# Optimization experiments

Hardware: AMD Instinct MI355X
Metric: run time of the kernel (lower is better)

The kernel has to match this reference:

```python
import jax, jax.numpy as jnp
import numpy as np
import math

NUM_HEADS = 8
DROPOUT_RATE = 0.1
D_IN = 32
D_PROJ = 32 * 16  # 512
B, SQ, SK = 8, 2048, 2048


def setup_inputs() -> dict:
    key = jax.random.key(0)
    ks = jax.random.split(key, 10)
    inv = 1.0 / math.sqrt(D_IN)
    return {
        "query": jax.random.normal(ks[0], (B, SQ, D_IN), dtype=jnp.float32),
        "key": jax.random.normal(ks[1], (B, SK, D_IN), dtype=jnp.float32),
        "value": jax.random.normal(ks[2], (B, SK, D_IN), dtype=jnp.float32),
        "mask": jax.random.randint(ks[3], (B, 1, 1, SK), 0, 2, dtype=jnp.int32),
        "Wq": jax.random.normal(ks[4], (D_PROJ, D_IN), dtype=jnp.float32) * inv,
        "bq": jax.random.normal(ks[5], (D_PROJ,), dtype=jnp.float32) * 0.02,
        "Wk": jax.random.normal(ks[6], (D_PROJ, D_IN), dtype=jnp.float32) * inv,
        "bk": jax.random.normal(ks[7], (D_PROJ,), dtype=jnp.float32) * 0.02,
        "Wv": jax.random.normal(ks[8], (D_PROJ, D_IN), dtype=jnp.float32) * inv,
        "bv": jax.random.normal(ks[9], (D_PROJ,), dtype=jnp.float32) * 0.02,
    }


def _split_heads(x):
    # [B, S, H*D] -> [B, H, S, D]
    b, s, _ = x.shape
    return x.reshape(b, s, NUM_HEADS, D_PROJ // NUM_HEADS).transpose(0, 2, 1, 3)


def reference(query, key, value, mask, Wq, bq, Wk, bk, Wv, bv):
    q = _split_heads(query @ Wq.T + bq)   # [B, H, Sq, D]
    k = _split_heads(key @ Wk.T + bk)     # [B, H, Sk, D]
    v = _split_heads(value @ Wv.T + bv)   # [B, H, Sk, D]

    head_dim = q.shape[-1]
    # mask only feeds this scalar; max(1-p, (1-p)/(Sm2*Sm3)) == 1-p for Sm2*Sm3 >= 1
    keep = 1.0 - DROPOUT_RATE
    scale_factor = jnp.maximum(jnp.float32(keep),
                               jnp.float32(keep / (mask.shape[2] * mask.shape[3])))

    scores = jnp.einsum("bhqd,bhkd->bhqk", q, k) * (scale_factor / math.sqrt(head_dim))
    probs = jax.nn.softmax(scores, axis=-1)
    # dropout treated as identity (eval mode) for a deterministic reference
    out = jnp.einsum("bhqk,bhkd->bhqd", probs, v)  # [B, H, Sq, D]
    b, h, sq, d = out.shape
    return out.transpose(0, 2, 1, 3).reshape(b, sq, h * d)
```

## Files before the change

### kernel.cpp

```cpp
#include <hip/hip_runtime.h>
#include <hip/hip_bf16.h>
#include <math.h>

#define B_   8
#define H_   8
#define S_   2048
#define D_   64
#define BH_  64
#define DPROJ_ 512

typedef __attribute__((ext_vector_type(8)))  _Float16 f16x8;
typedef __attribute__((ext_vector_type(4)))  float    f32x4;
typedef __attribute__((ext_vector_type(16))) float    f32x16;
typedef __attribute__((ext_vector_type(4)))  int      i32x4;

static __device__ __forceinline__ short f16bits(float f) {
    return __builtin_bit_cast(short, (_Float16)f);
}

static __device__ __forceinline__ f16x8 load8_f32_f16(const float* p) {
    const float4 a = ((const float4*)p)[0];
    const float4 b = ((const float4*)p)[1];
    f16x8 r;
    r[0] = (_Float16)a.x; r[1] = (_Float16)a.y; r[2] = (_Float16)a.z; r[3] = (_Float16)a.w;
    r[4] = (_Float16)b.x; r[5] = (_Float16)b.y; r[6] = (_Float16)b.z; r[7] = (_Float16)b.w;
    return r;
}

#if __has_builtin(__builtin_amdgcn_exp2f)
#define EXP2(x) __builtin_amdgcn_exp2f(x)
#else
#define EXP2(x) exp2f(x)
#endif

static __device__ __forceinline__ void pl32swap(unsigned int& a, unsigned int& b) {
#if __has_builtin(__builtin_amdgcn_permlane32_swap)
    auto r = __builtin_amdgcn_permlane32_swap((int)a, (int)b, false, false);
    a = (unsigned int)r[0];
    b = (unsigned int)r[1];
#else
    const bool lh0 = ((threadIdx.x & 63) < 32);
    unsigned int xa = (unsigned int)__shfl_xor((int)a, 32);
    unsigned int xb = (unsigned int)__shfl_xor((int)b, 32);
    unsigned int na = lh0 ? a : xb;
    unsigned int nb = lh0 ? xa : b;
    a = na; b = nb;
#endif
}

#define QKST 520

__global__ __launch_bounds__(256)
void proj_kernel(const float* __restrict__ query, const float* __restrict__ key,
                 const float* __restrict__ value,
                 const float* __restrict__ Wq, const float* __restrict__ bq,
                 const float* __restrict__ Wk, const float* __restrict__ bk,
                 const float* __restrict__ Wv, const float* __restrict__ bv,
                 short* __restrict__ qws, short* __restrict__ kws,
                 short* __restrict__ vws)
{
    __shared__ __align__(16) short shbuf[16384];

    const int tid  = threadIdx.x;
    const int wave = tid >> 6;
    const int lane = tid & 63;
    const int n    = lane & 15;
    const int quad = lane >> 4;
    const int kind = blockIdx.y;

    if (kind < 2) {
        short* tile = shbuf;
        const int r0   = blockIdx.x * 16;
        const int b    = r0 >> 11;
        const int s0   = r0 & 2047;
        const float QS = 0.16230319188537014f;

        const float* X    = kind ? key : query;
        const float* W    = kind ? Wk  : Wq;
        const float* bias = kind ? bk  : bq;
        short*       ows  = kind ? kws : qws;

        f16x8 af = load8_f32_f16(X + (r0 + n) * 32 + quad * 8);
        #pragma unroll
        for (int i = 0; i < 8; ++i) {
            const int c0 = wave * 128 + i * 16;
            f16x8 bfr = load8_f32_f16(W + (c0 + n) * 32 + quad * 8);
            f32x4 acc = {0.f, 0.f, 0.f, 0.f};
            acc = __builtin_amdgcn_mfma_f32_16x16x32_f16(af, bfr, acc, 0, 0, 0);
            const int c = c0 + n;
            const float bsf = bias[c];
            #pragma unroll
            for (int r = 0; r < 4; ++r) {
                float v = acc[r] + bsf;
                if (kind == 0) v *= QS;
                tile[(quad * 4 + r) * QKST + c] = f16bits(v);
            }
        }
        __syncthreads();

        #pragma unroll
        for (int k = 0; k < 4; ++k) {
            const int slot = k * 256 + tid;
            const int li   = slot & 7;
            const int chunk= slot >> 3;
            const int row  = chunk & 15;
            const int h    = chunk >> 4;
            uint4 vv = *(const uint4*)(tile + row * QKST + h * 64 + li * 8);
            *(uint4*)(ows + ((size_t)(b * 8 + h) * S_ + s0 + row) * 64 + li * 8) = vv;
        }
    } else {
        if (blockIdx.x >= 256) return;
        short* vtile = shbuf;
        const int r0   = blockIdx.x * 64;
        const int b    = r0 >> 11;
        const int s0   = r0 & 2047;
        const int sub  = wave >> 1;
        const int sh   = (wave & 1) * 16;

        #pragma unroll
        for (int half = 0; half < 2; ++half) {
            const int cbh = half * 256;
            f16x8 bfr = load8_f32_f16(value + (r0 + sub * 32 + sh + n) * 32 + quad * 8);
            #pragma unroll
            for (int i = 0; i < 16; ++i) {
                const int c0 = cbh + i * 16;
                f16x8 af = load8_f32_f16(Wv + (c0 + n) * 32 + quad * 8);
                f32x4 acc = {0.f, 0.f, 0.f, 0.f};
                acc = __builtin_amdgcn_mfma_f32_16x16x32_f16(af, bfr, acc, 0, 0, 0);
                #pragma unroll
                for (int r = 0; r < 4; ++r) {
                    const int dc = c0 + quad * 4 + r;
                    float v = acc[r] + bv[dc];
                    vtile[(sub * 256 + (dc - cbh)) * 32 + sh + n] = f16bits(v);
                }
            }
            __syncthreads();

            #pragma unroll
            for (int k = 0; k < 8; ++k) {
                const int slot = k * 256 + tid;
                const int li   = slot & 3;
                const int cl   = (slot >> 2) & 255;
                const int sb   = slot >> 10;
                const int c    = cbh + cl;
                const int bh   = b * 8 + (c >> 6);
                const int d    = c & 63;
                const int stile= (s0 >> 5) + sb;
                uint4 vv = *(const uint4*)(vtile + (sb * 256 + cl) * 32 + li * 8);
                *(uint4*)(vws + (((size_t)bh * (S_ / 32) + stile) * 64 + d) * 32 + li * 8) = vv;
            }
            if (half == 0) __syncthreads();
        }
    }
}

#define KST 72
#define VST 40
#define OTS 36

__global__ __launch_bounds__(256, 3)
void flash_kernel(const short* __restrict__ qws, const short* __restrict__ kws,
                  const short* __restrict__ vws, float* __restrict__ out)
{
    __shared__ __align__(16) short ldsk[2 * 32 * KST];
    __shared__ __align__(16) short ldsv[2 * 64 * VST];
    __shared__ __align__(16) float olds[4 * 32 * OTS];

    const int tid  = threadIdx.x;
    const int wave = tid >> 6;
    const int lane = tid & 63;
    const int m32  = lane & 31;
    const int lh   = lane >> 5;
    const int koff = lh * 8;
    const int bh   = blockIdx.x;
    const int q0   = blockIdx.y * 256 + wave * 64;

    const short* qbase = qws + (size_t)bh * S_ * D_;
    const short* kbase = kws + (size_t)bh * S_ * D_;
    const short* vbase = vws + (size_t)bh * (S_ / 32) * 2048;

    short* kdst0 = ldsk + (tid >> 3) * KST + (tid & 7) * 8;
    short* vdst0 = ldsv + (tid >> 2) * VST + (tid & 3) * 8;

    f16x8 qb[2][4];
    #pragma unroll
    for (int qg = 0; qg < 2; ++qg)
        #pragma unroll
        for (int h = 0; h < 4; ++h)
            qb[qg][h] = *(const f16x8*)(qbase + (q0 + qg * 32 + m32) * D_ + h * 16 + koff);

    f32x16 z16;
    #pragma unroll
    for (int r = 0; r < 16; ++r) z16[r] = 0.f;

    f32x16 o[2][2];
    float  pl[2] = {0.f, 0.f};
    #pragma unroll
    for (int qg = 0; qg < 2; ++qg)
        #pragma unroll
        for (int t = 0; t < 2; ++t)
            o[qg][t] = z16;

    {
        uint4 kr = *(const uint4*)(kbase + (size_t)tid * 8);
        uint4 vr = *(const uint4*)(vbase + (size_t)tid * 8);
        *(uint4*)kdst0 = kr;
        *(uint4*)vdst0 = vr;
    }
    __syncthreads();

    for (int it = 0; it < 64; ++it) {
        const int cur = it & 1, nx = cur ^ 1;

        uint4 kr, vr;
        if (it < 63) {
            kr = *(const uint4*)(kbase + (size_t)(it + 1) * 2048 + tid * 8);
            vr = *(const uint4*)(vbase + (size_t)(it + 1) * 2048 + tid * 8);
        }

        const short* kl = ldsk + cur * (32 * KST);
        const short* vl = ldsv + cur * (64 * VST);
        f16x8 kf[4], va[4];
        #pragma unroll
        for (int h = 0; h < 4; ++h)
            kf[h] = *(const f16x8*)(kl + m32 * KST + h * 16 + koff);
        #pragma unroll
        for (int t = 0; t < 2; ++t)
            #pragma unroll
            for (int kh = 0; kh < 2; ++kh)
                va[t * 2 + kh] = *(const f16x8*)(vl + (t * 32 + m32) * VST + kh * 16 + koff);

        #pragma unroll
        for (int qg = 0; qg < 2; ++qg) {
            f32x16 st = __builtin_amdgcn_mfma_f32_32x32x16_f16(kf[0], qb[qg][0], z16, 0, 0, 0);
            #pragma unroll
            for (int h = 1; h < 4; ++h)
                st = __builtin_amdgcn_mfma_f32_32x32x16_f16(kf[h], qb[qg][h], st, 0, 0, 0);

            float p[16];
            #pragma unroll
            for (int r = 0; r < 16; ++r) p[r] = EXP2(st[r]);
            float s01 = (p[0]+p[1]) + (p[2]+p[3]);
            float s23 = (p[4]+p[5]) + (p[6]+p[7]);
            float s45 = (p[8]+p[9]) + (p[10]+p[11]);
            float s67 = (p[12]+p[13]) + (p[14]+p[15]);
            pl[qg] += (s01 + s23) + (s45 + s67);

            unsigned int pk[8];
            #pragma unroll
            for (int i = 0; i < 8; ++i)
                pk[i] = __builtin_bit_cast(unsigned int,
                          __builtin_amdgcn_cvt_pkrtz(p[2 * i], p[2 * i + 1]));
            pl32swap(pk[0], pk[2]);
            pl32swap(pk[1], pk[3]);
            pl32swap(pk[4], pk[6]);
            pl32swap(pk[5], pk[7]);

            i32x4 bi0, bi1;
            bi0[0] = (int)pk[0]; bi0[1] = (int)pk[1];
            bi0[2] = (int)pk[2]; bi0[3] = (int)pk[3];
            bi1[0] = (int)pk[4]; bi1[1] = (int)pk[5];
            bi1[2] = (int)pk[6]; bi1[3] = (int)pk[7];
            f16x8 bf0 = __builtin_bit_cast(f16x8, bi0);
            f16x8 bf1 = __builtin_bit_cast(f16x8, bi1);

            #pragma unroll
            for (int t = 0; t < 2; ++t) {
                o[qg][t] = __builtin_amdgcn_mfma_f32_32x32x16_f16(va[t * 2 + 0], bf0, o[qg][t], 0, 0, 0);
                o[qg][t] = __builtin_amdgcn_mfma_f32_32x32x16_f16(va[t * 2 + 1], bf1, o[qg][t], 0, 0, 0);
            }
        }

        if (it < 63) {
            *(uint4*)(kdst0 + nx * (32 * KST)) = kr;
            *(uint4*)(vdst0 + nx * (64 * VST)) = vr;
        }
        __syncthreads();
    }

    const int b = bh >> 3, h = bh & 7;
    float* ow = olds + wave * (32 * OTS);
    #pragma unroll
    for (int qg = 0; qg < 2; ++qg) {
        float rs = pl[qg] + __shfl_xor(pl[qg], 32);
        float rl = 1.0f / rs;
        #pragma unroll
        for (int t = 0; t < 2; ++t) {
            const f32x16& ot = o[qg][t];
            #pragma unroll
            for (int g = 0; g < 4; ++g) {
                f32x4 w;
                w[0] = ot[g * 4 + 0] * rl;
                w[1] = ot[g * 4 + 1] * rl;
                w[2] = ot[g * 4 + 2] * rl;
                w[3] = ot[g * 4 + 3] * rl;
                *(f32x4*)(ow + m32 * OTS + 8 * g + 4 * lh) = w;
            }
            #pragma unroll
            for (int c = 0; c < 4; ++c) {
                const int row = (lane >> 3) + 8 * c;
                f32x4 v = *(const f32x4*)(ow + row * OTS + (lane & 7) * 4);
                const int sq = q0 + qg * 32 + row;
                *(f32x4*)(out + ((size_t)(b * S_ + sq)) * DPROJ_
                              + h * 64 + t * 32 + (lane & 7) * 4) = v;
            }
        }
    }
}

extern "C" void kernel_launch(void* const* d_in, const int* in_sizes, int n_in,
                              void* d_out, int out_size, void* d_ws, size_t ws_size,
                              hipStream_t stream)
{
    const float* query = (const float*)d_in[0];
    const float* key   = (const float*)d_in[1];
    const float* value = (const float*)d_in[2];
    const float* Wq = (const float*)d_in[4];
    const float* bq = (const float*)d_in[5];
    const float* Wk = (const float*)d_in[6];
    const float* bk = (const float*)d_in[7];
    const float* Wv = (const float*)d_in[8];
    const float* bv = (const float*)d_in[9];

    float* out = (float*)d_out;
    short* ws  = (short*)d_ws;
    const size_t TSZ = (size_t)BH_ * S_ * D_;
    short* qws = ws;
    short* kws = ws + TSZ;
    short* vws = ws + 2 * TSZ;

    proj_kernel<<<dim3((B_ * S_) / 16, 3), 256, 0, stream>>>(
        query, key, value, Wq, bq, Wk, bk, Wv, bv, qws, kws, vws);
    flash_kernel<<<dim3(BH_, S_ / 256), 256, 0, stream>>>(qws, kws, vws, out);
}
```

Measured before the change: 188.9 us.

## Triple-buffer K/V in LDS and register-prefetch next tile fragments

Turns the double-buffered K/V LDS pipeline into a three-stage ring. Global loads are issued two iterations ahead, and the next tile's K/V fragments are read from LDS into registers while the current tile's MFMAs run. The loop is unrolled by two so the register fragment sets can alternate. The aim is to hide global and LDS latency behind compute. In exchange it uses more LDS and registers, and launch bounds drop occupancy from 3 to 2 blocks per CU.

```diff
diff --git a/kernel.cpp b/kernel.cpp
--- a/kernel.cpp
+++ b/kernel.cpp
@@ -158,12 +158,97 @@
 #define VST 40
 #define OTS 36
 
-__global__ __launch_bounds__(256, 3)
+static __device__ __forceinline__ void flash_step(
+    int it,
+    const short* __restrict__ kbase, const short* __restrict__ vbase,
+    const short* ldsk, const short* ldsv,
+    short* kdst0, short* vdst0,
+    int m32, int koff, int tid,
+    int& rOff, int& wOff, int& fOff,
+    f16x8 (&kfc)[4], f16x8 (&vac)[4],
+    f16x8 (&kfn)[4], f16x8 (&van)[4],
+    const f16x8 (&qb)[2][4], const f32x16& z16,
+    f32x16 (&o)[2][2], float (&pl)[2])
+{
+    const bool doStage = (it < 62);
+    const bool doNext  = (it < 63);
+
+    uint4 kr, vr;
+    if (doStage) {
+        const size_t tb = (size_t)(it + 2) * 2048 + tid * 8;
+        kr = *(const uint4*)(kbase + tb);
+        vr = *(const uint4*)(vbase + tb);
+    }
+
+    if (doNext) {
+        const short* kl = ldsk + rOff * (32 * KST);
+        const short* vl = ldsv + rOff * (64 * VST);
+        #pragma unroll
+        for (int h = 0; h < 4; ++h)
+            kfn[h] = *(const f16x8*)(kl + m32 * KST + h * 16 + koff);
+        #pragma unroll
+        for (int t = 0; t < 2; ++t)
+            #pragma unroll
+            for (int kh = 0; kh < 2; ++kh)
+                van[t * 2 + kh] = *(const f16x8*)(vl + (t * 32 + m32) * VST + kh * 16 + koff);
+    }
+
+    #pragma unroll
+    for (int qg = 0; qg < 2; ++qg) {
+        f32x16 st = __builtin_amdgcn_mfma_f32_32x32x16_f16(kfc[0], qb[qg][0], z16, 0, 0, 0);
+        #pragma unroll
+        for (int h = 1; h < 4; ++h)
+            st = __builtin_amdgcn_mfma_f32_32x32x16_f16(kfc[h], qb[qg][h], st, 0, 0, 0);
+
+        float p[16];
+        #pragma unroll
+        for (int r = 0; r < 16; ++r) p[r] = EXP2(st[r]);
+        float s01 = (p[0]+p[1]) + (p[2]+p[3]);
+        float s23 = (p[4]+p[5]) + (p[6]+p[7]);
+        float s45 = (p[8]+p[9]) + (p[10]+p[11]);
+        float s67 = (p[12]+p[13]) + (p[14]+p[15]);
+        pl[qg] += (s01 + s23) + (s45 + s67);
+
+        unsigned int pk[8];
+        #pragma unroll
+        for (int i = 0; i < 8; ++i)
+            pk[i] = __builtin_bit_cast(unsigned int,
+                      __builtin_amdgcn_cvt_pkrtz(p[2 * i], p[2 * i + 1]));
+        pl32swap(pk[0], pk[2]);
+        pl32swap(pk[1], pk[3]);
+        pl32swap(pk[4], pk[6]);
+        pl32swap(pk[5], pk[7]);
+
+        i32x4 bi0, bi1;
+        bi0[0] = (int)pk[0]; bi0[1] = (int)pk[1];
+        bi0[2] = (int)pk[2]; bi0[3] = (int)pk[3];
+        bi1[0] = (int)pk[4]; bi1[1] = (int)pk[5];
+        bi1[2] = (int)pk[6]; bi1[3] = (int)pk[7];
+        f16x8 bf0 = __builtin_bit_cast(f16x8, bi0);
+        f16x8 bf1 = __builtin_bit_cast(f16x8, bi1);
+
+        #pragma unroll
+        for (int t = 0; t < 2; ++t) {
+            o[qg][t] = __builtin_amdgcn_mfma_f32_32x32x16_f16(vac[t * 2 + 0], bf0, o[qg][t], 0, 0, 0);
+            o[qg][t] = __builtin_amdgcn_mfma_f32_32x32x16_f16(vac[t * 2 + 1], bf1, o[qg][t], 0, 0, 0);
+        }
+    }
+
+    if (doStage) {
+        *(uint4*)(kdst0 + wOff * (32 * KST)) = kr;
+        *(uint4*)(vdst0 + wOff * (64 * VST)) = vr;
+    }
+    __syncthreads();
+
+    int t_ = fOff; fOff = rOff; rOff = wOff; wOff = t_;
+}
+
+__global__ __launch_bounds__(256, 2)
 void flash_kernel(const short* __restrict__ qws, const short* __restrict__ kws,
                   const short* __restrict__ vws, float* __restrict__ out)
 {
-    __shared__ __align__(16) short ldsk[2 * 32 * KST];
-    __shared__ __align__(16) short ldsv[2 * 64 * VST];
+    __shared__ __align__(16) short ldsk[3 * 32 * KST];
+    __shared__ __align__(16) short ldsv[3 * 64 * VST];
     __shared__ __align__(16) float olds[4 * 32 * OTS];
 
     const int tid  = threadIdx.x;
@@ -202,80 +287,36 @@
             o[qg][t] = z16;
 
     {
-        uint4 kr = *(const uint4*)(kbase + (size_t)tid * 8);
-        uint4 vr = *(const uint4*)(vbase + (size_t)tid * 8);
-        *(uint4*)kdst0 = kr;
-        *(uint4*)vdst0 = vr;
+        uint4 k0 = *(const uint4*)(kbase + (size_t)tid * 8);
+        uint4 v0 = *(const uint4*)(vbase + (size_t)tid * 8);
+        uint4 k1 = *(const uint4*)(kbase + (size_t)2048 + tid * 8);
+        uint4 v1 = *(const uint4*)(vbase + (size_t)2048 + tid * 8);
+        *(uint4*)kdst0 = k0;
+        *(uint4*)vdst0 = v0;
+        *(uint4*)(kdst0 + 32 * KST) = k1;
+        *(uint4*)(vdst0 + 64 * VST) = v1;
     }
     __syncthreads();
 
-    for (int it = 0; it < 64; ++it) {
-        const int cur = it & 1, nx = cur ^ 1;
-
-        uint4 kr, vr;
-        if (it < 63) {
-            kr = *(const uint4*)(kbase + (size_t)(it + 1) * 2048 + tid * 8);
-            vr = *(const uint4*)(vbase + (size_t)(it + 1) * 2048 + tid * 8);
-        }
-
-        const short* kl = ldsk + cur * (32 * KST);
-        const short* vl = ldsv + cur * (64 * VST);
-        f16x8 kf[4], va[4];
-        #pragma unroll
-        for (int h = 0; h < 4; ++h)
-            kf[h] = *(const f16x8*)(kl + m32 * KST + h * 16 + koff);
-        #pragma unroll
-        for (int t = 0; t < 2; ++t)
-            #pragma unroll
-            for (int kh = 0; kh < 2; ++kh)
-                va[t * 2 + kh] = *(const f16x8*)(vl + (t * 32 + m32) * VST + kh * 16 + koff);
-
-        #pragma unroll
-        for (int qg = 0; qg < 2; ++qg) {
-            f32x16 st = __builtin_amdgcn_mfma_f32_32x32x16_f16(kf[0], qb[qg][0], z16, 0, 0, 0);
-            #pragma unroll
-            for (int h = 1; h < 4; ++h)
-                st = __builtin_amdgcn_mfma_f32_32x32x16_f16(kf[h], qb[qg][h], st, 0, 0, 0);
-
-            float p[16];
-            #pragma unroll
-            for (int r = 0; r < 16; ++r) p[r] = EXP2(st[r]);
-            float s01 = (p[0]+p[1]) + (p[2]+p[3]);
-            float s23 = (p[4]+p[5]) + (p[6]+p[7]);
-            float s45 = (p[8]+p[9]) + (p[10]+p[11]);
-            float s67 = (p[12]+p[13]) + (p[14]+p[15]);
-            pl[qg] += (s01 + s23) + (s45 + s67);
-
-            unsigned int pk[8];
-            #pragma unroll
-            for (int i = 0; i < 8; ++i)
-                pk[i] = __builtin_bit_cast(unsigned int,
-                          __builtin_amdgcn_cvt_pkrtz(p[2 * i], p[2 * i + 1]));
-            pl32swap(pk[0], pk[2]);
-            pl32swap(pk[1], pk[3]);
-            pl32swap(pk[4], pk[6]);
-            pl32swap(pk[5], pk[7]);
-
-            i32x4 bi0, bi1;
-            bi0[0] = (int)pk[0]; bi0[1] = (int)pk[1];
-            bi0[2] = (int)pk[2]; bi0[3] = (int)pk[3];
-            bi1[0] = (int)pk[4]; bi1[1] = (int)pk[5];
-            bi1[2] = (int)pk[6]; bi1[3] = (int)pk[7];
-            f16x8 bf0 = __builtin_bit_cast(f16x8, bi0);
-            f16x8 bf1 = __builtin_bit_cast(f16x8, bi1);
-
-            #pragma unroll
-            for (int t = 0; t < 2; ++t) {
-                o[qg][t] = __builtin_amdgcn_mfma_f32_32x32x16_f16(va[t * 2 + 0], bf0, o[qg][t], 0, 0, 0);
-                o[qg][t] = __builtin_amdgcn_mfma_f32_32x32x16_f16(va[t * 2 + 1], bf1, o[qg][t], 0, 0, 0);
-            }
-        }
-
-        if (it < 63) {
-            *(uint4*)(kdst0 + nx * (32 * KST)) = kr;
-            *(uint4*)(vdst0 + nx * (64 * VST)) = vr;
-        }
-        __syncthreads();
+    f16x8 kfA[4], vaA[4], kfB[4], vaB[4];
+    #pragma unroll
+    for (int h = 0; h < 4; ++h)
+        kfA[h] = *(const f16x8*)(ldsk + m32 * KST + h * 16 + koff);
+    #pragma unroll
+    for (int t = 0; t < 2; ++t)
+        #pragma unroll
+        for (int kh = 0; kh < 2; ++kh)
+            vaA[t * 2 + kh] = *(const f16x8*)(ldsv + (t * 32 + m32) * VST + kh * 16 + koff);
+
+    int rOff = 1, wOff = 2, fOff = 0;
+
+    for (int it = 0; it < 64; it += 2) {
+        flash_step(it,     kbase, vbase, ldsk, ldsv, kdst0, vdst0,
+                   m32, koff, tid, rOff, wOff, fOff,
+                   kfA, vaA, kfB, vaB, qb, z16, o, pl);
+        flash_step(it + 1, kbase, vbase, ldsk, ldsv, kdst0, vdst0,
+                   m32, koff, tid, rOff, wOff, fOff,
+                   kfB, vaB, kfA, vaA, qb, z16, o, pl);
     }
 
     const int b = bh >> 3, h = bh & 7;
```

After: 185.0 us. -2.0%, faster.

## Pre-swizzle K/V into MFMA fragment order and load directly from global memory

Applied to the files above, without the earlier changes.

The projection kernel now writes K and V into a fragment-ordered layout so each lane can fetch its MFMA operands with contiguous 16-byte global loads. The flash kernel drops the LDS double buffer and its per-iteration __syncthreads, and instead register-double-buffers K/V fragments across two unrolled iterations. Launch bounds drop to 2 blocks per SM to leave room for the extra registers. Each wave now fetches K/V itself instead of sharing an LDS copy across the four waves, which raises L2 traffic and lowers occupancy.

```diff
diff --git a/kernel.cpp b/kernel.cpp
--- a/kernel.cpp
+++ b/kernel.cpp
@@ -104,9 +104,16 @@
             const int li   = slot & 7;
             const int chunk= slot >> 3;
             const int row  = chunk & 15;
-            const int h    = chunk >> 4;
-            uint4 vv = *(const uint4*)(tile + row * QKST + h * 64 + li * 8);
-            *(uint4*)(ows + ((size_t)(b * 8 + h) * S_ + s0 + row) * 64 + li * 8) = vv;
+            const int hd   = chunk >> 4;
+            uint4 vv = *(const uint4*)(tile + row * QKST + hd * 64 + li * 8);
+            const int bh = b * 8 + hd;
+            if (kind == 0) {
+                *(uint4*)(ows + ((size_t)bh * S_ + s0 + row) * 64 + li * 8) = vv;
+            } else {
+                const int s = s0 + row;
+                *(uint4*)(ows + (size_t)bh * (S_ * 64)
+                              + (size_t)(s >> 5) * 2048 + li * 256 + (s & 31) * 8) = vv;
+            }
         }
     } else {
         if (blockIdx.x >= 256) return;
@@ -147,23 +154,69 @@
                 const int d    = c & 63;
                 const int stile= (s0 >> 5) + sb;
                 uint4 vv = *(const uint4*)(vtile + (sb * 256 + cl) * 32 + li * 8);
-                *(uint4*)(vws + (((size_t)bh * (S_ / 32) + stile) * 64 + d) * 32 + li * 8) = vv;
+                *(uint4*)(vws + (size_t)bh * (S_ * 64)
+                              + (size_t)stile * 2048
+                              + ((d >> 5) * 4 + (li >> 1) * 2 + (li & 1)) * 256
+                              + (d & 31) * 8) = vv;
             }
             if (half == 0) __syncthreads();
         }
     }
 }
 
-#define KST 72
-#define VST 40
 #define OTS 36
 
-__global__ __launch_bounds__(256, 3)
+static __device__ __forceinline__ void flash_compute(
+    const f16x8 (&kf)[4], const f16x8 (&va)[4],
+    const f16x8 (&qb)[2][4], const f32x16& z16,
+    f32x16 (&o)[2][2], float (&pl)[2])
+{
+    #pragma unroll
+    for (int qg = 0; qg < 2; ++qg) {
+        f32x16 st = __builtin_amdgcn_mfma_f32_32x32x16_f16(kf[0], qb[qg][0], z16, 0, 0, 0);
+        #pragma unroll
+        for (int h = 1; h < 4; ++h)
+            st = __builtin_amdgcn_mfma_f32_32x32x16_f16(kf[h], qb[qg][h], st, 0, 0, 0);
+
+        float p[16];
+        #pragma unroll
+        for (int r = 0; r < 16; ++r) p[r] = EXP2(st[r]);
+        float s01 = (p[0]+p[1]) + (p[2]+p[3]);
+        float s23 = (p[4]+p[5]) + (p[6]+p[7]);
+        float s45 = (p[8]+p[9]) + (p[10]+p[11]);
+        float s67 = (p[12]+p[13]) + (p[14]+p[15]);
+        pl[qg] += (s01 + s23) + (s45 + s67);
+
+        unsigned int pk[8];
+        #pragma unroll
+        for (int i = 0; i < 8; ++i)
+            pk[i] = __builtin_bit_cast(unsigned int,
+                      __builtin_amdgcn_cvt_pkrtz(p[2 * i], p[2 * i + 1]));
+        pl32swap(pk[0], pk[2]);
+        pl32swap(pk[1], pk[3]);
+        pl32swap(pk[4], pk[6]);
+        pl32swap(pk[5], pk[7]);
+
+        i32x4 bi0, bi1;
+        bi0[0] = (int)pk[0]; bi0[1] = (int)pk[1];
+        bi0[2] = (int)pk[2]; bi0[3] = (int)pk[3];
+        bi1[0] = (int)pk[4]; bi1[1] = (int)pk[5];
+        bi1[2] = (int)pk[6]; bi1[3] = (int)pk[7];
+        f16x8 bf0 = __builtin_bit_cast(f16x8, bi0);
+        f16x8 bf1 = __builtin_bit_cast(f16x8, bi1);
+
+        #pragma unroll
+        for (int t = 0; t < 2; ++t) {
+            o[qg][t] = __builtin_amdgcn_mfma_f32_32x32x16_f16(va[t * 2 + 0], bf0, o[qg][t], 0, 0, 0);
+            o[qg][t] = __builtin_amdgcn_mfma_f32_32x32x16_f16(va[t * 2 + 1], bf1, o[qg][t], 0, 0, 0);
+        }
+    }
+}
+
+__global__ __launch_bounds__(256, 2)
 void flash_kernel(const short* __restrict__ qws, const short* __restrict__ kws,
                   const short* __restrict__ vws, float* __restrict__ out)
 {
-    __shared__ __align__(16) short ldsk[2 * 32 * KST];
-    __shared__ __align__(16) short ldsv[2 * 64 * VST];
     __shared__ __align__(16) float olds[4 * 32 * OTS];
 
     const int tid  = threadIdx.x;
@@ -176,11 +229,9 @@
     const int q0   = blockIdx.y * 256 + wave * 64;
 
     const short* qbase = qws + (size_t)bh * S_ * D_;
-    const short* kbase = kws + (size_t)bh * S_ * D_;
-    const short* vbase = vws + (size_t)bh * (S_ / 32) * 2048;
-
-    short* kdst0 = ldsk + (tid >> 3) * KST + (tid & 7) * 8;
-    short* vdst0 = ldsv + (tid >> 2) * VST + (tid & 3) * 8;
+    const short* kfb   = kws + (size_t)bh * (S_ * 64);
+    const short* vfb   = vws + (size_t)bh * (S_ * 64);
+    const int loff = lh * 256 + m32 * 8;
 
     f16x8 qb[2][4];
     #pragma unroll
@@ -201,82 +252,30 @@
         for (int t = 0; t < 2; ++t)
             o[qg][t] = z16;
 
-    {
-        uint4 kr = *(const uint4*)(kbase + (size_t)tid * 8);
-        uint4 vr = *(const uint4*)(vbase + (size_t)tid * 8);
-        *(uint4*)kdst0 = kr;
-        *(uint4*)vdst0 = vr;
+    #define LOADFRAGS(T, kf, va) do {                                        \
+        const short* kp_ = kfb + (size_t)(T) * 2048 + loff;                  \
+        const short* vp_ = vfb + (size_t)(T) * 2048 + loff;                  \
+        kf[0] = *(const f16x8*)(kp_);                                        \
+        kf[1] = *(const f16x8*)(kp_ + 512);                                  \
+        kf[2] = *(const f16x8*)(kp_ + 1024);                                 \
+        kf[3] = *(const f16x8*)(kp_ + 1536);                                 \
+        va[0] = *(const f16x8*)(vp_);                                        \
+        va[1] = *(const f16x8*)(vp_ + 512);                                  \
+        va[2] = *(const f16x8*)(vp_ + 1024);                                 \
+        va[3] = *(const f16x8*)(vp_ + 1536);                                 \
+    } while (0)
+
+    f16x8 kfA[4], vaA[4], kfB[4], vaB[4];
+    LOADFRAGS(0, kfA, vaA);
+
+    for (int it = 0; it < 64; it += 2) {
+        LOADFRAGS(it + 1, kfB, vaB);
+        flash_compute(kfA, vaA, qb, z16, o, pl);
+        if (it + 2 < 64)
+            LOADFRAGS(it + 2, kfA, vaA);
+        flash_compute(kfB, vaB, qb, z16, o, pl);
     }
-    __syncthreads();
-
-    for (int it = 0; it < 64; ++it) {
-        const int cur = it & 1, nx = cur ^ 1;
-
-        uint4 kr, vr;
-        if (it < 63) {
-            kr = *(const uint4*)(kbase + (size_t)(it + 1) * 2048 + tid * 8);
-            vr = *(const uint4*)(vbase + (size_t)(it + 1) * 2048 + tid * 8);
-        }
-
-        const short* kl = ldsk + cur * (32 * KST);
-        const short* vl = ldsv + cur * (64 * VST);
-        f16x8 kf[4], va[4];
-        #pragma unroll
-        for (int h = 0; h < 4; ++h)
-            kf[h] = *(const f16x8*)(kl + m32 * KST + h * 16 + koff);
-        #pragma unroll
-        for (int t = 0; t < 2; ++t)
-            #pragma unroll
-            for (int kh = 0; kh < 2; ++kh)
-                va[t * 2 + kh] = *(const f16x8*)(vl + (t * 32 + m32) * VST + kh * 16 + koff);
-
-        #pragma unroll
-        for (int qg = 0; qg < 2; ++qg) {
-            f32x16 st = __builtin_amdgcn_mfma_f32_32x32x16_f16(kf[0], qb[qg][0], z16, 0, 0, 0);
-            #pragma unroll
-            for (int h = 1; h < 4; ++h)
-                st = __builtin_amdgcn_mfma_f32_32x32x16_f16(kf[h], qb[qg][h], st, 0, 0, 0);
-
-            float p[16];
-            #pragma unroll
-            for (int r = 0; r < 16; ++r) p[r] = EXP2(st[r]);
-            float s01 = (p[0]+p[1]) + (p[2]+p[3]);
-            float s23 = (p[4]+p[5]) + (p[6]+p[7]);
-            float s45 = (p[8]+p[9]) + (p[10]+p[11]);
-            float s67 = (p[12]+p[13]) + (p[14]+p[15]);
-            pl[qg] += (s01 + s23) + (s45 + s67);
-
-            unsigned int pk[8];
-            #pragma unroll
-            for (int i = 0; i < 8; ++i)
-                pk[i] = __builtin_bit_cast(unsigned int,
-                          __builtin_amdgcn_cvt_pkrtz(p[2 * i], p[2 * i + 1]));
-            pl32swap(pk[0], pk[2]);
-            pl32swap(pk[1], pk[3]);
-            pl32swap(pk[4], pk[6]);
-            pl32swap(pk[5], pk[7]);
-
-            i32x4 bi0, bi1;
-            bi0[0] = (int)pk[0]; bi0[1] = (int)pk[1];
-            bi0[2] = (int)pk[2]; bi0[3] = (int)pk[3];
-            bi1[0] = (int)pk[4]; bi1[1] = (int)pk[5];
-            bi1[2] = (int)pk[6]; bi1[3] = (int)pk[7];
-            f16x8 bf0 = __builtin_bit_cast(f16x8, bi0);
-            f16x8 bf1 = __builtin_bit_cast(f16x8, bi1);
-
-            #pragma unroll
-            for (int t = 0; t < 2; ++t) {
-                o[qg][t] = __builtin_amdgcn_mfma_f32_32x32x16_f16(va[t * 2 + 0], bf0, o[qg][t], 0, 0, 0);
-                o[qg][t] = __builtin_amdgcn_mfma_f32_32x32x16_f16(va[t * 2 + 1], bf1, o[qg][t], 0, 0, 0);
-            }
-        }
-
-        if (it < 63) {
-            *(uint4*)(kdst0 + nx * (32 * KST)) = kr;
-            *(uint4*)(vdst0 + nx * (64 * VST)) = vr;
-        }
-        __syncthreads();
-    }
+    #undef LOADFRAGS
 
     const int b = bh >> 3, h = bh & 7;
     float* ow = olds + wave * (32 * OTS);
```

After: 184.8 us. -2.1%, faster.
